# Performance work log

Hardware: AMD Instinct MI355X
Metric: run time of the kernel (lower is better)

## Reference

```python
import jax, jax.numpy as jnp
import numpy as np

N_NODES = 50000
N_EDGES = 800000
N_GRAPHS = 500
IN_DIM, HID, OUT = 128, 64, 10


def setup_inputs() -> dict:
    key = jax.random.key(0)
    ks = jax.random.split(key, 12)
    x = jax.random.normal(ks[0], (N_NODES, IN_DIM), dtype=jnp.float32)
    edge_index = jax.random.randint(ks[1], (2, N_EDGES), 0, N_NODES, dtype=jnp.int32)
    batch = jnp.sort(jax.random.randint(ks[2], (N_NODES,), 0, N_GRAPHS, dtype=jnp.int32))
    def glorot(k, shape):
        lim = np.sqrt(6.0 / (shape[0] + shape[1]))
        return jax.random.uniform(k, shape, jnp.float32, -lim, lim)
    return {
        "x": x, "edge_index": edge_index, "batch": batch,
        "W1": glorot(ks[3], (IN_DIM, HID)), "b1": jnp.zeros((HID,), jnp.float32),
        "W2": glorot(ks[4], (HID, HID)),    "b2": jnp.zeros((HID,), jnp.float32),
        "W3": glorot(ks[5], (HID, HID)),    "b3": jnp.zeros((HID,), jnp.float32),
        "lin_W1": glorot(ks[6], (HID, HID)), "lin_b1": jnp.zeros((HID,), jnp.float32),
        "lin_W2": glorot(ks[7], (HID, OUT)), "lin_b2": jnp.zeros((OUT,), jnp.float32),
    }


def _gcn_conv(x, src, dst, deg_inv_sqrt, W, b):
    # PyG GCNConv: h = x @ W, then sym-normalized scatter-add over edges (self-loops included in src/dst)
    h = x @ W                                   # [N, out]
    norm = deg_inv_sqrt[src] * deg_inv_sqrt[dst]  # [E+N]
    msgs = h[src] * norm[:, None]               # [E+N, out]  (large gathered intermediate)
    out = jax.ops.segment_sum(msgs, dst, num_segments=N_NODES)
    return out + b


def reference(x, edge_index, batch, W1, b1, W2, b2, W3, b3, lin_W1, lin_b1, lin_W2, lin_b2):
    # add self-loops once; degree (with edge weight 1) computed on target nodes
    loops = jnp.arange(N_NODES, dtype=edge_index.dtype)
    src = jnp.concatenate([edge_index[0], loops])
    dst = jnp.concatenate([edge_index[1], loops])
    deg = jax.ops.segment_sum(jnp.ones_like(dst, dtype=x.dtype), dst, num_segments=N_NODES)
    deg_inv_sqrt = jnp.where(deg > 0, jax.lax.rsqrt(jnp.maximum(deg, 1e-12)), 0.0)

    h = jax.nn.relu(_gcn_conv(x, src, dst, deg_inv_sqrt, W1, b1))
    h = jax.nn.relu(_gcn_conv(h, src, dst, deg_inv_sqrt, W2, b2))
    h = jax.nn.relu(_gcn_conv(h, src, dst, deg_inv_sqrt, W3, b3))

    # global mean pool over graphs
    sums = jax.ops.segment_sum(h, batch, num_segments=N_GRAPHS)
    counts = jax.ops.segment_sum(jnp.ones((h.shape[0],), h.dtype), batch, num_segments=N_GRAPHS)
    pooled = sums / jnp.maximum(counts, 1.0)[:, None]  # [G, HID]

    # MLP head (dropout p=0 / eval -> identity)
    logits = jax.nn.relu(pooled @ lin_W1 + lin_b1) @ lin_W2 + lin_b2
    return (logits, jnp.zeros((), x.dtype))
```

## Files before the change

kernel.cpp:

```cpp
#include <hip/hip_runtime.h>
#include <hip/hip_bf16.h>

#define N_NODES 50000
#define N_EDGES 800000
#define N_GRAPHS 500
#define IN_DIM 128
#define HID 64
#define OUT_DIM 10
#define NB_BUCK ((N_NODES + 63) >> 6)
#define NBLK 256
#define BLDT 256

__device__ __forceinline__ float bf2f(unsigned short u) {
    return __uint_as_float(((unsigned)u) << 16);
}
__device__ __forceinline__ unsigned short f2bf(float f) {
    unsigned x = __float_as_uint(f);
    x += 0x7fffu + ((x >> 16) & 1u);
    return (unsigned short)(x >> 16);
}

__global__ __launch_bounds__(BLDT) void p1_hist_kernel(const int* __restrict__ dst,
                                                       int* __restrict__ bhist, int e, int epb) {
    __shared__ int h[NB_BUCK];
    int tid = threadIdx.x;
    int blk = blockIdx.x;
    for (int i = tid; i < NB_BUCK; i += BLDT) h[i] = 0;
    __syncthreads();
    int e0 = blk * epb;
    int e1 = e0 + epb;
    if (e1 > e) e1 = e;
    int i = e0 + tid * 4;
    for (; i + 3 < e1; i += BLDT * 4) {
        int4 d4 = *(const int4*)&dst[i];
        atomicAdd(&h[d4.x >> 6], 1);
        atomicAdd(&h[d4.y >> 6], 1);
        atomicAdd(&h[d4.z >> 6], 1);
        atomicAdd(&h[d4.w >> 6], 1);
    }
    for (int k = i; k < e1 && k < i + 4; ++k) atomicAdd(&h[dst[k] >> 6], 1);
    __syncthreads();
    for (int j = tid; j < NB_BUCK; j += BLDT) bhist[blk * NB_BUCK + j] = h[j];
}

__global__ __launch_bounds__(NBLK) void scanA_kernel(int* __restrict__ bhist,
                                                     int* __restrict__ bsum) {
    __shared__ int s[NBLK];
    int b = blockIdx.x;
    int t = threadIdx.x;
    int c = bhist[t * NB_BUCK + b];
    s[t] = c;
    __syncthreads();
    for (int off = 1; off < NBLK; off <<= 1) {
        int x = (t >= off) ? s[t - off] : 0;
        __syncthreads();
        s[t] += x;
        __syncthreads();
    }
    bhist[t * NB_BUCK + b] = s[t] - c;
    if (t == NBLK - 1) bsum[b] = s[t];
}

__global__ __launch_bounds__(1024) void bscan_kernel(const int* __restrict__ bsum,
                                                     int* __restrict__ bstart, int nb, int e) {
    __shared__ int s[1024];
    int t = threadIdx.x;
    int v = (t < nb) ? bsum[t] : 0;
    s[t] = v;
    __syncthreads();
    for (int off = 1; off < 1024; off <<= 1) {
        int x = (t >= off) ? s[t - off] : 0;
        __syncthreads();
        s[t] += x;
        __syncthreads();
    }
    if (t < nb) bstart[t] = s[t] - v;
    if (t == 0) bstart[nb] = e;
}

__global__ __launch_bounds__(BLDT) void p2_place_kernel(
    const int* __restrict__ src, const int* __restrict__ dst, const int* __restrict__ bstart,
    const int* __restrict__ base, unsigned* __restrict__ pairs, int e, int epb) {
    __shared__ int h[NB_BUCK];
    __shared__ int sb[NB_BUCK];
    int tid = threadIdx.x;
    int blk = blockIdx.x;
    for (int i = tid; i < NB_BUCK; i += BLDT) {
        h[i] = 0;
        sb[i] = bstart[i] + base[blk * NB_BUCK + i];
    }
    __syncthreads();
    int e0 = blk * epb;
    int e1 = e0 + epb;
    if (e1 > e) e1 = e;
    int i = e0 + tid * 4;
    for (; i + 3 < e1; i += BLDT * 4) {
        int4 d4 = *(const int4*)&dst[i];
        int4 s4 = *(const int4*)&src[i];
        int b0 = d4.x >> 6, b1 = d4.y >> 6, b2 = d4.z >> 6, b3 = d4.w >> 6;
        int r0 = atomicAdd(&h[b0], 1);
        int r1 = atomicAdd(&h[b1], 1);
        int r2 = atomicAdd(&h[b2], 1);
        int r3 = atomicAdd(&h[b3], 1);
        pairs[sb[b0] + r0] = ((unsigned)(d4.x & 63) << 16) | (unsigned)s4.x;
        pairs[sb[b1] + r1] = ((unsigned)(d4.y & 63) << 16) | (unsigned)s4.y;
        pairs[sb[b2] + r2] = ((unsigned)(d4.z & 63) << 16) | (unsigned)s4.z;
        pairs[sb[b3] + r3] = ((unsigned)(d4.w & 63) << 16) | (unsigned)s4.w;
    }
    for (int k = i; k < e1 && k < i + 4; ++k) {
        int d = dst[k];
        int b = d >> 6;
        int r = atomicAdd(&h[b], 1);
        pairs[sb[b] + r] = ((unsigned)(d & 63) << 16) | (unsigned)src[k];
    }
}

__global__ __launch_bounds__(256) void csr_scatter2_kernel(
    const unsigned* __restrict__ pairs, const int* __restrict__ bstart,
    int* __restrict__ rs, float* __restrict__ dinv, int* __restrict__ csr_src, int n) {
    __shared__ int lcnt[64];
    __shared__ int lcur[64];
    int b = blockIdx.x;
    int tid = threadIdx.x;
    int beg = bstart[b], end = bstart[b + 1];
    if (tid < 64) lcnt[tid] = 0;
    __syncthreads();
    for (int i = beg + tid; i < end; i += 256) atomicAdd(&lcnt[pairs[i] >> 16], 1);
    __syncthreads();
    if (tid < 64) {
        int c = lcnt[tid];
        int v = c;
#pragma unroll
        for (int off = 1; off < 64; off <<= 1) {
            int t = __shfl_up(v, off);
            if (tid >= off) v += t;
        }
        int excl = v - c;
        int node = b * 64 + tid;
        if (node <= n) {
            rs[node] = beg + excl;
            if (node < n) dinv[node] = rsqrtf((float)(c + 1));
        }
        lcur[tid] = beg + excl;
    }
    __syncthreads();
    for (int i = beg + tid; i < end; i += 256) {
        unsigned p = pairs[i];
        int slot = atomicAdd(&lcur[p >> 16], 1);
        csr_src[slot] = (int)(p & 0xffffu);
    }
}

__global__ __launch_bounds__(256) void linear1_kernel(
    const float* __restrict__ A, const float* __restrict__ W,
    const float* __restrict__ dinv, unsigned short* __restrict__ C, int n) {
    const int K = IN_DIM;
    __shared__ float As[64][K + 4];
    __shared__ float Ws[K][64];
    int tid = threadIdx.x;
    int tx = tid & 15;
    int ty = tid >> 4;
    int block0 = blockIdx.x * 64;
    int rows = n - block0;
    if (rows > 64) rows = 64;

    const float* Abase = A + (size_t)block0 * K;
    int totalA4 = (rows * K) >> 2;
    for (int i4 = tid; i4 < totalA4; i4 += 256) {
        int i = i4 << 2;
        float4 v = *(const float4*)(Abase + i);
        *(float4*)&As[i / K][i % K] = v;
    }
    {
        const float4* Wv = (const float4*)W;
        float4* Wsv = (float4*)&Ws[0][0];
        for (int i = tid; i < K * 16; i += 256) Wsv[i] = Wv[i];
    }
    __syncthreads();

    float acc[4][4] = {};
#pragma unroll 2
    for (int k = 0; k < K; k += 4) {
        float4 a[4];
#pragma unroll
        for (int i = 0; i < 4; ++i) a[i] = *(const float4*)&As[ty * 4 + i][k];
        float4 w[4];
#pragma unroll
        for (int kk = 0; kk < 4; ++kk) w[kk] = *(const float4*)&Ws[k + kk][tx * 4];
#pragma unroll
        for (int i = 0; i < 4; ++i) {
            float av[4] = {a[i].x, a[i].y, a[i].z, a[i].w};
#pragma unroll
            for (int kk = 0; kk < 4; ++kk) {
                acc[i][0] += av[kk] * w[kk].x;
                acc[i][1] += av[kk] * w[kk].y;
                acc[i][2] += av[kk] * w[kk].z;
                acc[i][3] += av[kk] * w[kk].w;
            }
        }
    }

#pragma unroll
    for (int i = 0; i < 4; ++i) {
        int r = ty * 4 + i;
        if (r < rows) {
            float s = dinv[block0 + r];
            ushort4 v;
            v.x = f2bf(acc[i][0] * s);
            v.y = f2bf(acc[i][1] * s);
            v.z = f2bf(acc[i][2] * s);
            v.w = f2bf(acc[i][3] * s);
            *(ushort4*)&C[(size_t)(block0 + r) * 64 + tx * 4] = v;
        }
    }
}

__global__ __launch_bounds__(256) void linear_bf_kernel(
    const unsigned short* __restrict__ A, const float* __restrict__ W,
    const float* __restrict__ dinv, unsigned short* __restrict__ C, int n) {
    const int K = HID;
    __shared__ float As[64][K + 4];
    __shared__ float Ws[K][64];
    int tid = threadIdx.x;
    int tx = tid & 15;
    int ty = tid >> 4;
    int block0 = blockIdx.x * 64;
    int rows = n - block0;
    if (rows > 64) rows = 64;

    const unsigned short* Abase = A + (size_t)block0 * K;
    int total8 = rows * 8;
    for (int u = tid; u < total8; u += 256) {
        int r = u >> 3;
        int c8 = (u & 7) << 3;
        uint4 raw = *(const uint4*)(Abase + (size_t)r * K + c8);
        float4 a0, a1;
        a0.x = __uint_as_float(raw.x << 16);
        a0.y = __uint_as_float(raw.x & 0xffff0000u);
        a0.z = __uint_as_float(raw.y << 16);
        a0.w = __uint_as_float(raw.y & 0xffff0000u);
        a1.x = __uint_as_float(raw.z << 16);
        a1.y = __uint_as_float(raw.z & 0xffff0000u);
        a1.z = __uint_as_float(raw.w << 16);
        a1.w = __uint_as_float(raw.w & 0xffff0000u);
        *(float4*)&As[r][c8] = a0;
        *(float4*)&As[r][c8 + 4] = a1;
    }
    {
        const float4* Wv = (const float4*)W;
        float4* Wsv = (float4*)&Ws[0][0];
        for (int i = tid; i < K * 16; i += 256) Wsv[i] = Wv[i];
    }
    __syncthreads();

    float acc[4][4] = {};
#pragma unroll 2
    for (int k = 0; k < K; k += 4) {
        float4 a[4];
#pragma unroll
        for (int i = 0; i < 4; ++i) a[i] = *(const float4*)&As[ty * 4 + i][k];
        float4 w[4];
#pragma unroll
        for (int kk = 0; kk < 4; ++kk) w[kk] = *(const float4*)&Ws[k + kk][tx * 4];
#pragma unroll
        for (int i = 0; i < 4; ++i) {
            float av[4] = {a[i].x, a[i].y, a[i].z, a[i].w};
#pragma unroll
            for (int kk = 0; kk < 4; ++kk) {
                acc[i][0] += av[kk] * w[kk].x;
                acc[i][1] += av[kk] * w[kk].y;
                acc[i][2] += av[kk] * w[kk].z;
                acc[i][3] += av[kk] * w[kk].w;
            }
        }
    }

#pragma unroll
    for (int i = 0; i < 4; ++i) {
        int r = ty * 4 + i;
        if (r < rows) {
            float s = dinv[block0 + r];
            ushort4 v;
            v.x = f2bf(acc[i][0] * s);
            v.y = f2bf(acc[i][1] * s);
            v.z = f2bf(acc[i][2] * s);
            v.w = f2bf(acc[i][3] * s);
            *(ushort4*)&C[(size_t)(block0 + r) * 64 + tx * 4] = v;
        }
    }
}

__global__ __launch_bounds__(256) void gather_kernel(
    const unsigned short* __restrict__ hs, const int* __restrict__ rs,
    const int* __restrict__ csr_src, const float* __restrict__ dinv,
    const float* __restrict__ bias, unsigned short* __restrict__ outp, int n) {
    int wave = threadIdx.x >> 6;
    int node = blockIdx.x * 4 + wave;
    if (node >= n) return;
    int lane = threadIdx.x & 63;
    int eg = lane >> 4;
    int f4 = (lane & 15) << 2;
    int beg = rs[node], end = rs[node + 1];
    int len = end - beg;
    int q = (len + 3) >> 2;
    int mb = beg + eg * q;
    int me = mb + q;
    if (me > end) me = end;
    float4 acc = {0.f, 0.f, 0.f, 0.f};
    if (eg == 0) {
        ushort4 u = *(const ushort4*)&hs[(size_t)node * 64 + f4];
        acc.x = bf2f(u.x); acc.y = bf2f(u.y); acc.z = bf2f(u.z); acc.w = bf2f(u.w);
    }
    int j = mb;
    for (; j + 3 < me; j += 4) {
        int s0 = csr_src[j];
        int s1 = csr_src[j + 1];
        int s2 = csr_src[j + 2];
        int s3 = csr_src[j + 3];
        ushort4 u0 = *(const ushort4*)&hs[(size_t)s0 * 64 + f4];
        ushort4 u1 = *(const ushort4*)&hs[(size_t)s1 * 64 + f4];
        ushort4 u2 = *(const ushort4*)&hs[(size_t)s2 * 64 + f4];
        ushort4 u3 = *(const ushort4*)&hs[(size_t)s3 * 64 + f4];
        acc.x += bf2f(u0.x) + bf2f(u1.x) + bf2f(u2.x) + bf2f(u3.x);
        acc.y += bf2f(u0.y) + bf2f(u1.y) + bf2f(u2.y) + bf2f(u3.y);
        acc.z += bf2f(u0.z) + bf2f(u1.z) + bf2f(u2.z) + bf2f(u3.z);
        acc.w += bf2f(u0.w) + bf2f(u1.w) + bf2f(u2.w) + bf2f(u3.w);
    }
    if (j + 1 < me) {
        int s0 = csr_src[j];
        int s1 = csr_src[j + 1];
        ushort4 u0 = *(const ushort4*)&hs[(size_t)s0 * 64 + f4];
        ushort4 u1 = *(const ushort4*)&hs[(size_t)s1 * 64 + f4];
        acc.x += bf2f(u0.x) + bf2f(u1.x);
        acc.y += bf2f(u0.y) + bf2f(u1.y);
        acc.z += bf2f(u0.z) + bf2f(u1.z);
        acc.w += bf2f(u0.w) + bf2f(u1.w);
        j += 2;
    }
    if (j < me) {
        int s = csr_src[j];
        ushort4 u = *(const ushort4*)&hs[(size_t)s * 64 + f4];
        acc.x += bf2f(u.x); acc.y += bf2f(u.y); acc.z += bf2f(u.z); acc.w += bf2f(u.w);
    }
    acc.x += __shfl_xor(acc.x, 16); acc.y += __shfl_xor(acc.y, 16);
    acc.z += __shfl_xor(acc.z, 16); acc.w += __shfl_xor(acc.w, 16);
    acc.x += __shfl_xor(acc.x, 32); acc.y += __shfl_xor(acc.y, 32);
    acc.z += __shfl_xor(acc.z, 32); acc.w += __shfl_xor(acc.w, 32);
    if (eg == 0) {
        float s = dinv[node];
        float4 bb = *(const float4*)&bias[f4];
        ushort4 o;
        o.x = f2bf(fmaxf(acc.x * s + bb.x, 0.f));
        o.y = f2bf(fmaxf(acc.y * s + bb.y, 0.f));
        o.z = f2bf(fmaxf(acc.z * s + bb.z, 0.f));
        o.w = f2bf(fmaxf(acc.w * s + bb.w, 0.f));
        *(ushort4*)&outp[(size_t)node * 64 + f4] = o;
    }
}

__device__ __forceinline__ int lower_bound_dev(const int* __restrict__ a, int n, int v) {
    int lo = 0, hi = n;
    while (lo < hi) {
        int m = (lo + hi) >> 1;
        if (a[m] < v) lo = m + 1; else hi = m;
    }
    return lo;
}

__global__ __launch_bounds__(256) void pool_head_kernel(
    const unsigned short* __restrict__ h, const int* __restrict__ batch,
    const float* __restrict__ W1, const float* __restrict__ b1,
    const float* __restrict__ W2, const float* __restrict__ b2,
    float* __restrict__ out, int nNodes, int nGraphs) {
    __shared__ float psum[4][64];
    __shared__ float p[64];
    __shared__ float t64[64];
    int g = blockIdx.x;
    int tid = threadIdx.x;
    int f = tid & 63;
    int q = tid >> 6;
    int lo = lower_bound_dev(batch, nNodes, g);
    int hi = lower_bound_dev(batch, nNodes, g + 1);
    float sum = 0.0f;
    for (int i = lo + q; i < hi; i += 4) sum += bf2f(h[(size_t)i * 64 + f]);
    psum[q][f] = sum;
    __syncthreads();
    if (tid < 64) {
        float s = psum[0][f] + psum[1][f] + psum[2][f] + psum[3][f];
        float inv = 1.0f / fmaxf((float)(hi - lo), 1.0f);
        p[f] = s * inv;
        float acc = b1[f];
#pragma unroll
        for (int k = 0; k < 64; ++k) acc += p[k] * W1[k * 64 + f];
        t64[f] = fmaxf(acc, 0.0f);
        if (f < OUT_DIM) {
            float acc2 = b2[f];
#pragma unroll
            for (int k = 0; k < 64; ++k) acc2 += t64[k] * W2[k * OUT_DIM + f];
            out[g * OUT_DIM + f] = acc2;
        }
        if (g == 0 && f == 0) out[nGraphs * OUT_DIM] = 0.0f;
    }
}

extern "C" void kernel_launch(void* const* d_in, const int* in_sizes, int n_in,
                              void* d_out, int out_size, void* d_ws, size_t ws_size,
                              hipStream_t stream) {
    const float* x      = (const float*)d_in[0];
    const int*   eidx   = (const int*)d_in[1];
    const int*   batch  = (const int*)d_in[2];
    const float* W1     = (const float*)d_in[3];
    const float* b1     = (const float*)d_in[4];
    const float* W2     = (const float*)d_in[5];
    const float* b2     = (const float*)d_in[6];
    const float* W3     = (const float*)d_in[7];
    const float* b3     = (const float*)d_in[8];
    const float* lin_W1 = (const float*)d_in[9];
    const float* lin_b1 = (const float*)d_in[10];
    const float* lin_W2 = (const float*)d_in[11];
    const float* lin_b2 = (const float*)d_in[12];
    float* out = (float*)d_out;

    const int E = in_sizes[1] / 2;
    const int N = N_NODES;
    const int NF = N * HID;
    int epb = (E + NBLK - 1) / NBLK;
    epb = (epb + 7) & ~7;

    const int* src = eidx;
    const int* dst = eidx + E;

    unsigned short* buf1 = (unsigned short*)d_ws;
    unsigned short* buf2 = buf1 + NF;
    float* dinv = (float*)(buf2 + NF);
    int* bhist  = (int*)(dinv + N);
    int* bsum   = bhist + NBLK * NB_BUCK;
    int* bstart = bsum + NB_BUCK;
    int* rs     = bstart + NB_BUCK + 1;
    int* csr_src = rs + N + 1;
    unsigned* pairs = (unsigned*)(csr_src + E);

    const int TILES = (N + 63) / 64;
    const int GBLK = (N + 3) / 4;

    p1_hist_kernel<<<NBLK, BLDT, 0, stream>>>(dst, bhist, E, epb);
    scanA_kernel<<<NB_BUCK, NBLK, 0, stream>>>(bhist, bsum);
    bscan_kernel<<<1, 1024, 0, stream>>>(bsum, bstart, NB_BUCK, E);
    p2_place_kernel<<<NBLK, BLDT, 0, stream>>>(src, dst, bstart, bhist, pairs, E, epb);
    csr_scatter2_kernel<<<NB_BUCK, 256, 0, stream>>>(pairs, bstart, rs, dinv, csr_src, N);

    linear1_kernel<<<TILES, 256, 0, stream>>>(x, W1, dinv, buf1, N);
    gather_kernel<<<GBLK, 256, 0, stream>>>(buf1, rs, csr_src, dinv, b1, buf2, N);

    linear_bf_kernel<<<TILES, 256, 0, stream>>>(buf2, W2, dinv, buf1, N);
    gather_kernel<<<GBLK, 256, 0, stream>>>(buf1, rs, csr_src, dinv, b2, buf2, N);

    linear_bf_kernel<<<TILES, 256, 0, stream>>>(buf2, W3, dinv, buf1, N);
    gather_kernel<<<GBLK, 256, 0, stream>>>(buf1, rs, csr_src, dinv, b3, buf2, N);

    pool_head_kernel<<<N_GRAPHS, 256, 0, stream>>>(buf2, batch, lin_W1, lin_b1, lin_W2, lin_b2,
                                                   out, N, N_GRAPHS);
}
```

Baseline: 254.9 us.

## Fuse bucket scan into placement, CSR build into first linear, widen gather loads

Drops the separate single-block bucket-offset scan by having every placement block redundantly scan the bucket sums, with block 0 writing bucket starts. Merges the CSR scatter kernel with the first linear layer so one launch builds the per-node CSR and computes the X·W1 tile, reading degree scale from shared memory. The gather kernel now loads 8 bf16 features per lane (16B) with 8 edge groups instead of 4, which means more shuffle reductions. Launches drop by two, at the cost of redundant scan work and a heavier fused kernel.

```diff
diff --git a/kernel.cpp b/kernel.cpp
--- a/kernel.cpp
+++ b/kernel.cpp
@@ -18,6 +18,16 @@
     unsigned x = __float_as_uint(f);
     x += 0x7fffu + ((x >> 16) & 1u);
     return (unsigned short)(x >> 16);
+}
+__device__ __forceinline__ void acc8(float a[8], uint4 r) {
+    a[0] += __uint_as_float(r.x << 16);
+    a[1] += __uint_as_float(r.x & 0xffff0000u);
+    a[2] += __uint_as_float(r.y << 16);
+    a[3] += __uint_as_float(r.y & 0xffff0000u);
+    a[4] += __uint_as_float(r.z << 16);
+    a[5] += __uint_as_float(r.z & 0xffff0000u);
+    a[6] += __uint_as_float(r.w << 16);
+    a[7] += __uint_as_float(r.w & 0xffff0000u);
 }
 
 __global__ __launch_bounds__(BLDT) void p1_hist_kernel(const int* __restrict__ dst,
@@ -61,33 +71,47 @@
     if (t == NBLK - 1) bsum[b] = s[t];
 }
 
-__global__ __launch_bounds__(1024) void bscan_kernel(const int* __restrict__ bsum,
-                                                     int* __restrict__ bstart, int nb, int e) {
-    __shared__ int s[1024];
-    int t = threadIdx.x;
-    int v = (t < nb) ? bsum[t] : 0;
-    s[t] = v;
-    __syncthreads();
-    for (int off = 1; off < 1024; off <<= 1) {
-        int x = (t >= off) ? s[t - off] : 0;
-        __syncthreads();
-        s[t] += x;
-        __syncthreads();
-    }
-    if (t < nb) bstart[t] = s[t] - v;
-    if (t == 0) bstart[nb] = e;
-}
-
 __global__ __launch_bounds__(BLDT) void p2_place_kernel(
-    const int* __restrict__ src, const int* __restrict__ dst, const int* __restrict__ bstart,
-    const int* __restrict__ base, unsigned* __restrict__ pairs, int e, int epb) {
+    const int* __restrict__ src, const int* __restrict__ dst,
+    const int* __restrict__ bsum, const int* __restrict__ base,
+    unsigned* __restrict__ pairs, int* __restrict__ bstart, int e, int epb) {
     __shared__ int h[NB_BUCK];
     __shared__ int sb[NB_BUCK];
+    __shared__ int ts[BLDT];
     int tid = threadIdx.x;
     int blk = blockIdx.x;
-    for (int i = tid; i < NB_BUCK; i += BLDT) {
-        h[i] = 0;
-        sb[i] = bstart[i] + base[blk * NB_BUCK + i];
+    int i0 = tid << 2;
+    int v0 = 0, v1 = 0, v2 = 0, v3 = 0;
+    if (i0 < NB_BUCK) v0 = bsum[i0];
+    if (i0 + 1 < NB_BUCK) v1 = bsum[i0 + 1];
+    if (i0 + 2 < NB_BUCK) v2 = bsum[i0 + 2];
+    if (i0 + 3 < NB_BUCK) v3 = bsum[i0 + 3];
+    int tsum = v0 + v1 + v2 + v3;
+    ts[tid] = tsum;
+    for (int i = tid; i < NB_BUCK; i += BLDT) h[i] = 0;
+    __syncthreads();
+    for (int off = 1; off < BLDT; off <<= 1) {
+        int x = (tid >= off) ? ts[tid - off] : 0;
+        __syncthreads();
+        ts[tid] += x;
+        __syncthreads();
+    }
+    int excl = ts[tid] - tsum;
+    int s0 = excl;
+    int s1 = s0 + v0;
+    int s2 = s1 + v1;
+    int s3 = s2 + v2;
+    const int* bb = base + blk * NB_BUCK;
+    if (i0 < NB_BUCK) sb[i0] = s0 + bb[i0];
+    if (i0 + 1 < NB_BUCK) sb[i0 + 1] = s1 + bb[i0 + 1];
+    if (i0 + 2 < NB_BUCK) sb[i0 + 2] = s2 + bb[i0 + 2];
+    if (i0 + 3 < NB_BUCK) sb[i0 + 3] = s3 + bb[i0 + 3];
+    if (blk == 0) {
+        if (i0 < NB_BUCK) bstart[i0] = s0;
+        if (i0 + 1 < NB_BUCK) bstart[i0 + 1] = s1;
+        if (i0 + 2 < NB_BUCK) bstart[i0 + 2] = s2;
+        if (i0 + 3 < NB_BUCK) bstart[i0 + 3] = s3;
+        if (tid == 0) bstart[NB_BUCK] = e;
     }
     __syncthreads();
     int e0 = blk * epb;
@@ -115,11 +139,17 @@
     }
 }
 
-__global__ __launch_bounds__(256) void csr_scatter2_kernel(
+__global__ __launch_bounds__(256) void csr_lin1_kernel(
     const unsigned* __restrict__ pairs, const int* __restrict__ bstart,
-    int* __restrict__ rs, float* __restrict__ dinv, int* __restrict__ csr_src, int n) {
+    int* __restrict__ rs, float* __restrict__ dinv, int* __restrict__ csr_src,
+    const float* __restrict__ A, const float* __restrict__ W,
+    unsigned short* __restrict__ C, int n) {
+    const int K = IN_DIM;
+    __shared__ float As[64][K + 4];
+    __shared__ float Ws[K][64];
     __shared__ int lcnt[64];
     __shared__ int lcur[64];
+    __shared__ float sdinv[64];
     int b = blockIdx.x;
     int tid = threadIdx.x;
     int beg = bstart[b], end = bstart[b + 1];
@@ -137,10 +167,12 @@
         }
         int excl = v - c;
         int node = b * 64 + tid;
+        float dv = rsqrtf((float)(c + 1));
         if (node <= n) {
             rs[node] = beg + excl;
-            if (node < n) dinv[node] = rsqrtf((float)(c + 1));
-        }
+            if (node < n) dinv[node] = dv;
+        }
+        sdinv[tid] = dv;
         lcur[tid] = beg + excl;
     }
     __syncthreads();
@@ -149,18 +181,8 @@
         int slot = atomicAdd(&lcur[p >> 16], 1);
         csr_src[slot] = (int)(p & 0xffffu);
     }
-}
-
-__global__ __launch_bounds__(256) void linear1_kernel(
-    const float* __restrict__ A, const float* __restrict__ W,
-    const float* __restrict__ dinv, unsigned short* __restrict__ C, int n) {
-    const int K = IN_DIM;
-    __shared__ float As[64][K + 4];
-    __shared__ float Ws[K][64];
-    int tid = threadIdx.x;
-    int tx = tid & 15;
-    int ty = tid >> 4;
-    int block0 = blockIdx.x * 64;
+
+    int block0 = b * 64;
     int rows = n - block0;
     if (rows > 64) rows = 64;
 
@@ -178,6 +200,8 @@
     }
     __syncthreads();
 
+    int tx = tid & 15;
+    int ty = tid >> 4;
     float acc[4][4] = {};
 #pragma unroll 2
     for (int k = 0; k < K; k += 4) {
@@ -204,7 +228,7 @@
     for (int i = 0; i < 4; ++i) {
         int r = ty * 4 + i;
         if (r < rows) {
-            float s = dinv[block0 + r];
+            float s = sdinv[r];
             ushort4 v;
             v.x = f2bf(acc[i][0] * s);
             v.y = f2bf(acc[i][1] * s);
@@ -298,18 +322,18 @@
     int node = blockIdx.x * 4 + wave;
     if (node >= n) return;
     int lane = threadIdx.x & 63;
-    int eg = lane >> 4;
-    int f4 = (lane & 15) << 2;
+    int eg = lane >> 3;
+    int f8 = (lane & 7) << 3;
     int beg = rs[node], end = rs[node + 1];
     int len = end - beg;
-    int q = (len + 3) >> 2;
+    int q = (len + 7) >> 3;
     int mb = beg + eg * q;
     int me = mb + q;
     if (me > end) me = end;
-    float4 acc = {0.f, 0.f, 0.f, 0.f};
+    float a[8] = {0.f, 0.f, 0.f, 0.f, 0.f, 0.f, 0.f, 0.f};
     if (eg == 0) {
-        ushort4 u = *(const ushort4*)&hs[(size_t)node * 64 + f4];
-        acc.x = bf2f(u.x); acc.y = bf2f(u.y); acc.z = bf2f(u.z); acc.w = bf2f(u.w);
+        uint4 r = *(const uint4*)&hs[(size_t)node * 64 + f8];
+        acc8(a, r);
     }
     int j = mb;
     for (; j + 3 < me; j += 4) {
@@ -317,44 +341,53 @@
         int s1 = csr_src[j + 1];
         int s2 = csr_src[j + 2];
         int s3 = csr_src[j + 3];
-        ushort4 u0 = *(const ushort4*)&hs[(size_t)s0 * 64 + f4];
-        ushort4 u1 = *(const ushort4*)&hs[(size_t)s1 * 64 + f4];
-        ushort4 u2 = *(const ushort4*)&hs[(size_t)s2 * 64 + f4];
-        ushort4 u3 = *(const ushort4*)&hs[(size_t)s3 * 64 + f4];
-        acc.x += bf2f(u0.x) + bf2f(u1.x) + bf2f(u2.x) + bf2f(u3.x);
-        acc.y += bf2f(u0.y) + bf2f(u1.y) + bf2f(u2.y) + bf2f(u3.y);
-        acc.z += bf2f(u0.z) + bf2f(u1.z) + bf2f(u2.z) + bf2f(u3.z);
-        acc.w += bf2f(u0.w) + bf2f(u1.w) + bf2f(u2.w) + bf2f(u3.w);
+        uint4 r0 = *(const uint4*)&hs[(size_t)s0 * 64 + f8];
+        uint4 r1 = *(const uint4*)&hs[(size_t)s1 * 64 + f8];
+        uint4 r2 = *(const uint4*)&hs[(size_t)s2 * 64 + f8];
+        uint4 r3 = *(const uint4*)&hs[(size_t)s3 * 64 + f8];
+        acc8(a, r0);
+        acc8(a, r1);
+        acc8(a, r2);
+        acc8(a, r3);
     }
     if (j + 1 < me) {
         int s0 = csr_src[j];
         int s1 = csr_src[j + 1];
-        ushort4 u0 = *(const ushort4*)&hs[(size_t)s0 * 64 + f4];
-        ushort4 u1 = *(const ushort4*)&hs[(size_t)s1 * 64 + f4];
-        acc.x += bf2f(u0.x) + bf2f(u1.x);
-        acc.y += bf2f(u0.y) + bf2f(u1.y);
-        acc.z += bf2f(u0.z) + bf2f(u1.z);
-        acc.w += bf2f(u0.w) + bf2f(u1.w);
+        uint4 r0 = *(const uint4*)&hs[(size_t)s0 * 64 + f8];
+        uint4 r1 = *(const uint4*)&hs[(size_t)s1 * 64 + f8];
+        acc8(a, r0);
+        acc8(a, r1);
         j += 2;
     }
     if (j < me) {
-        int s = csr_src[j];
-        ushort4 u = *(const ushort4*)&hs[(size_t)s * 64 + f4];
-        acc.x += bf2f(u.x); acc.y += bf2f(u.y); acc.z += bf2f(u.z); acc.w += bf2f(u.w);
-    }
-    acc.x += __shfl_xor(acc.x, 16); acc.y += __shfl_xor(acc.y, 16);
-    acc.z += __shfl_xor(acc.z, 16); acc.w += __shfl_xor(acc.w, 16);
-    acc.x += __shfl_xor(acc.x, 32); acc.y += __shfl_xor(acc.y, 32);
-    acc.z += __shfl_xor(acc.z, 32); acc.w += __shfl_xor(acc.w, 32);
+        int s0 = csr_src[j];
+        uint4 r0 = *(const uint4*)&hs[(size_t)s0 * 64 + f8];
+        acc8(a, r0);
+    }
+#pragma unroll
+    for (int k = 0; k < 8; ++k) a[k] += __shfl_xor(a[k], 8);
+#pragma unroll
+    for (int k = 0; k < 8; ++k) a[k] += __shfl_xor(a[k], 16);
+#pragma unroll
+    for (int k = 0; k < 8; ++k) a[k] += __shfl_xor(a[k], 32);
     if (eg == 0) {
         float s = dinv[node];
-        float4 bb = *(const float4*)&bias[f4];
-        ushort4 o;
-        o.x = f2bf(fmaxf(acc.x * s + bb.x, 0.f));
-        o.y = f2bf(fmaxf(acc.y * s + bb.y, 0.f));
-        o.z = f2bf(fmaxf(acc.z * s + bb.z, 0.f));
-        o.w = f2bf(fmaxf(acc.w * s + bb.w, 0.f));
-        *(ushort4*)&outp[(size_t)node * 64 + f4] = o;
+        float4 b0 = *(const float4*)&bias[f8];
+        float4 b1 = *(const float4*)&bias[f8 + 4];
+        float v0 = fmaxf(a[0] * s + b0.x, 0.f);
+        float v1 = fmaxf(a[1] * s + b0.y, 0.f);
+        float v2 = fmaxf(a[2] * s + b0.z, 0.f);
+        float v3 = fmaxf(a[3] * s + b0.w, 0.f);
+        float v4 = fmaxf(a[4] * s + b1.x, 0.f);
+        float v5 = fmaxf(a[5] * s + b1.y, 0.f);
+        float v6 = fmaxf(a[6] * s + b1.z, 0.f);
+        float v7 = fmaxf(a[7] * s + b1.w, 0.f);
+        uint4 o;
+        o.x = (unsigned)f2bf(v0) | ((unsigned)f2bf(v1) << 16);
+        o.y = (unsigned)f2bf(v2) | ((unsigned)f2bf(v3) << 16);
+        o.z = (unsigned)f2bf(v4) | ((unsigned)f2bf(v5) << 16);
+        o.w = (unsigned)f2bf(v6) | ((unsigned)f2bf(v7) << 16);
+        *(uint4*)&outp[(size_t)node * 64 + f8] = o;
     }
 }
 
@@ -445,11 +478,10 @@
 
     p1_hist_kernel<<<NBLK, BLDT, 0, stream>>>(dst, bhist, E, epb);
     scanA_kernel<<<NB_BUCK, NBLK, 0, stream>>>(bhist, bsum);
-    bscan_kernel<<<1, 1024, 0, stream>>>(bsum, bstart, NB_BUCK, E);
-    p2_place_kernel<<<NBLK, BLDT, 0, stream>>>(src, dst, bstart, bhist, pairs, E, epb);
-    csr_scatter2_kernel<<<NB_BUCK, 256, 0, stream>>>(pairs, bstart, rs, dinv, csr_src, N);
-
-    linear1_kernel<<<TILES, 256, 0, stream>>>(x, W1, dinv, buf1, N);
+    p2_place_kernel<<<NBLK, BLDT, 0, stream>>>(src, dst, bsum, bhist, pairs, bstart, E, epb);
+
+    csr_lin1_kernel<<<TILES, 256, 0, stream>>>(pairs, bstart, rs, dinv, csr_src,
+                                               x, W1, buf1, N);
     gather_kernel<<<GBLK, 256, 0, stream>>>(buf1, rs, csr_src, dinv, b1, buf2, N);
 
     linear_bf_kernel<<<TILES, 256, 0, stream>>>(buf2, W2, dinv, buf1, N);
```

New measurement: 246.5 us. 1.03x faster.
